# Kernel tuning notes

Measured on AMD Instinct MI355X. Metric: run time of the kernel, lower is better.

The kernel has to match this reference:

```python
import jax, jax.numpy as jnp
import numpy as np

B, N_EX, N_KC, D_E, D_C, D_H = 32, 1024, 128, 64, 64, 64


def setup_inputs() -> dict:
    key = jax.random.key(0)
    ks = jax.random.split(key, 20)
    return {
        "h": jax.random.normal(ks[0], (B, N_KC, D_H), jnp.float32),
        "ex": jax.random.uniform(ks[1], (B, N_EX), jnp.float32),
        "su": jax.random.uniform(ks[2], (B,), jnp.float32),
        "ex_graph": jax.random.uniform(ks[3], (N_EX, N_KC), jnp.float32),
        "kc_gamma": jax.random.normal(ks[4], (N_KC, N_KC), jnp.float32),
        "W_ex": jax.random.normal(ks[5], (D_E, 2 * N_EX), jnp.float32) * 0.02,
        "W_kc": jax.random.normal(ks[6], (D_C, N_KC), jnp.float32) * 0.05,
        "tgru_wih": jax.random.normal(ks[7], (3 * D_H, D_E), jnp.float32) * 0.05,
        "tgru_whh": jax.random.normal(ks[8], (3 * D_H, D_H), jnp.float32) * 0.05,
        "tgru_bih": jax.random.normal(ks[9], (3 * D_H,), jnp.float32) * 0.05,
        "tgru_bhh": jax.random.normal(ks[10], (3 * D_H,), jnp.float32) * 0.05,
        "fpart_w": jax.random.normal(ks[11], (D_H, D_C + D_H), jnp.float32) * 0.05,
        "fpart_b": jax.random.normal(ks[12], (D_H,), jnp.float32) * 0.05,
        "ulin_w": jax.random.normal(ks[13], (D_H, D_H), jnp.float32) * 0.05,
        "ulin_b": jax.random.normal(ks[14], (D_H,), jnp.float32) * 0.05,
        "ugru_wih": jax.random.normal(ks[15], (3 * D_H, D_H), jnp.float32) * 0.05,
        "ugru_whh": jax.random.normal(ks[16], (3 * D_H, D_H), jnp.float32) * 0.05,
        "ugru_bih": jax.random.normal(ks[17], (3 * D_H,), jnp.float32) * 0.05,
        "ugru_bhh": jax.random.normal(ks[18], (3 * D_H,), jnp.float32) * 0.05,
    }


def _gru_cell(x, h, wih, whh, bih, bhh):
    # torch.nn.GRUCell: gates in order r, z, n
    gi = x @ wih.T + bih
    gh = h @ whh.T + bhh
    ir, iz, inn = jnp.split(gi, 3, axis=-1)
    hr, hz, hn = jnp.split(gh, 3, axis=-1)
    r = jax.nn.sigmoid(ir + hr)
    z = jax.nn.sigmoid(iz + hz)
    n = jnp.tanh(inn + r * hn)
    return (1.0 - z) * n + z * h


def reference(h, ex, su, ex_graph, kc_gamma, W_ex, W_kc,
              tgru_wih, tgru_whh, tgru_bih, tgru_bhh,
              fpart_w, fpart_b, ulin_w, ulin_b,
              ugru_wih, ugru_whh, ugru_bih, ugru_bhh):
    bsz, n_kc, d_h = h.shape
    kc_graph = jax.nn.sigmoid(kc_gamma)  # (n_kc, n_kc)

    # exercise embedding from [ex*su, ex*(1-su)]
    x_id = jnp.concatenate([ex * su[:, None], ex * (1.0 - su)[:, None]], axis=-1)  # (B, 2*n_ex)
    x = x_id @ W_ex.T  # (B, d_e)

    kci = ex @ ex_graph  # (B, n_kc)
    kci_flat = kci.reshape(bsz * n_kc, 1)

    # temporal GRU update, gated by kci
    x_rep = jnp.broadcast_to(x[:, None, :], (bsz, n_kc, x.shape[-1])).reshape(bsz * n_kc, -1)
    h_flat = h.reshape(bsz * n_kc, d_h)
    th = _gru_cell(x_rep, h_flat, tgru_wih, tgru_whh, tgru_bih, tgru_bhh)
    new_h = (1.0 - kci_flat) * h_flat + kci_flat * th  # (B*n_kc, d_h)

    delta_h = (new_h - h_flat).reshape(bsz, n_kc, d_h)

    # kc_embeddings(eye(n_kc)) == W_kc.T : (n_kc, d_c)
    e = W_kc.T
    # fpart(concat([delta_h_i, e_j])) split into the two weight blocks
    W_dh = fpart_w[:, :d_h]   # acts on delta_h
    W_e = fpart_w[:, d_h:]    # acts on e
    dpart = delta_h @ W_dh.T                      # (B, n_kc_i, d_h)
    epart = e @ W_e.T + fpart_b                   # (n_kc_j, d_h)
    pre = dpart[:, :, None, :] + epart[None, None, :, :]  # (B, i, j, d_h)
    partij = jax.nn.relu(pre)
    partij = partij * kc_graph[None, :, :, None] * kci[:, :, None, None]
    partj = jnp.sum(partij, axis=1)               # (B, n_kc_j, d_h)

    outj = jax.nn.relu(partj @ ulin_w.T + ulin_b).reshape(bsz * n_kc, d_h)
    kcj = (kci @ kc_graph).reshape(bsz * n_kc, 1)

    uh = _gru_cell(outj, new_h, ugru_wih, ugru_whh, ugru_bih, ugru_bhh)
    h_out = (1.0 - kcj) * new_h + kcj * uh
    return h_out.reshape(bsz, n_kc, d_h)
```

## Files before the change

kernel.cpp:

```cpp
#include <hip/hip_runtime.h>
#include <math.h>

#define NB  32
#define NKC 128
#define DH  64
#define NEX 1024
#define G3  192

#define XOFF    0
#define KCIOFF  2048
#define NHOFF   6144
#define DPOFF   268288

__device__ __forceinline__ float sigf(float x) { return 1.0f / (1.0f + expf(-x)); }
__device__ __forceinline__ float dot4(float4 a, float4 b) {
    return fmaf(a.x, b.x, fmaf(a.y, b.y, fmaf(a.z, b.z, a.w * b.w)));
}

__global__ __launch_bounds__(256) void k0_x(
    const float* __restrict__ ex, const float* __restrict__ su,
    const float* __restrict__ W_ex, float* __restrict__ ws)
{
    int t = threadIdx.x, wave = t >> 6, lane = t & 63;
    int b = blockIdx.x >> 3;
    int dbase = (blockIdx.x & 7) * 8;
    float sub = su[b];
    const float* exb = ex + (size_t)b * NEX;
    float er[16];
    #pragma unroll
    for (int i = 0; i < 16; ++i) er[i] = exb[lane + i * 64];
    #pragma unroll
    for (int p = 0; p < 2; ++p) {
        int d = dbase + wave * 2 + p;
        const float* wr = W_ex + (size_t)d * (2 * NEX);
        float a1 = 0.f, a2 = 0.f;
        #pragma unroll
        for (int i = 0; i < 16; ++i) {
            int k = lane + i * 64;
            a1 = fmaf(er[i], wr[k], a1);
            a2 = fmaf(er[i], wr[NEX + k], a2);
        }
        float v = sub * a1 + (1.0f - sub) * a2;
        #pragma unroll
        for (int off = 32; off; off >>= 1) v += __shfl_down(v, off, 64);
        if (lane == 0) ws[XOFF + b * DH + d] = v;
    }
}

__global__ __launch_bounds__(512) void k1_tgru(
    const float* __restrict__ h, const float* __restrict__ ex,
    const float* __restrict__ ex_graph,
    const float* __restrict__ tgru_wih, const float* __restrict__ tgru_whh,
    const float* __restrict__ tgru_bih, const float* __restrict__ tgru_bhh,
    const float* __restrict__ fpart_w, float* __restrict__ ws)
{
    int t = threadIdx.x, wave = t >> 6, lane = t & 63;
    int b = blockIdx.x >> 3;
    int i0 = (blockIdx.x & 7) * 16;

    __shared__ __align__(16) float whh68[G3 * 36];
    __shared__ __align__(16) float wih68[G3 * 36];
    __shared__ __align__(16) float ht[16 * DH];
    __shared__ __align__(16) float dlt[16 * DH];
    __shared__ __align__(16) float xs[DH];
    __shared__ float kred[512];
    __shared__ float gis[G3];
    __shared__ float bhh3[G3];
    __shared__ float kciL[16];

    {
        int i = t & 15, ks = t >> 4, kb = ks * 32;
        const float* exb = ex + (size_t)b * NEX;
        const float* eg = ex_graph + i0 + i;
        float a = 0.f;
        #pragma unroll 4
        for (int k = 0; k < 32; ++k)
            a = fmaf(exb[kb + k], eg[(size_t)(kb + k) * NKC], a);
        kred[t] = a;
    }
    const float* hb = h + (size_t)(b * NKC + i0) * DH;
    for (int idx = t; idx < 16 * DH; idx += 512) ht[idx] = hb[idx];
    if (t < DH) xs[t] = ws[XOFF + b * DH + t];
    if (t < G3) bhh3[t] = tgru_bhh[t];
    __syncthreads();
    if (t < 16) {
        float s = 0.f;
        #pragma unroll
        for (int r = 0; r < 32; ++r) s += kred[r * 16 + t];
        kciL[t] = s;
        ws[KCIOFF + b * NKC + i0 + t] = s;
    }

    float giA = (t < G3) ? tgru_bih[t] : 0.f;
    float ar[2], az[2], an[2];
    #pragma unroll
    for (int m = 0; m < 2; ++m) {
        ar[m] = bhh3[lane]; az[m] = bhh3[64 + lane]; an[m] = bhh3[128 + lane];
    }
    for (int ch = 0; ch < 2; ++ch) {
        __syncthreads();
        for (int idx = t; idx < G3 * 8; idx += 512) {
            int row = idx >> 3, q = idx & 7;
            *(float4*)&whh68[row * 36 + 4 * q] =
                *(const float4*)&tgru_whh[row * DH + ch * 32 + 4 * q];
            *(float4*)&wih68[row * 36 + 4 * q] =
                *(const float4*)&tgru_wih[row * DH + ch * 32 + 4 * q];
        }
        __syncthreads();
        if (t < G3) {
            #pragma unroll
            for (int q = 0; q < 8; ++q) {
                float4 wv = *(float4*)&wih68[t * 36 + 4 * q];
                float4 xv = *(float4*)&xs[ch * 32 + 4 * q];
                giA += dot4(wv, xv);
            }
        }
        #pragma unroll
        for (int q = 0; q < 8; ++q) {
            float4 wr = *(float4*)&whh68[lane * 36 + 4 * q];
            float4 wz = *(float4*)&whh68[(64 + lane) * 36 + 4 * q];
            float4 wn = *(float4*)&whh68[(128 + lane) * 36 + 4 * q];
            int kb = ch * 32 + 4 * q;
            #pragma unroll
            for (int m = 0; m < 2; ++m) {
                float4 hk = *(float4*)&ht[(wave * 2 + m) * DH + kb];
                ar[m] += dot4(wr, hk);
                az[m] += dot4(wz, hk);
                an[m] += dot4(wn, hk);
            }
        }
    }
    if (t < G3) gis[t] = giA;
    __syncthreads();
    #pragma unroll
    for (int m = 0; m < 2; ++m) {
        int il = wave * 2 + m;
        float hval = ht[il * DH + lane];
        float r = sigf(gis[lane] + ar[m]);
        float z = sigf(gis[64 + lane] + az[m]);
        float n = tanhf(gis[128 + lane] + r * an[m]);
        float th = (1.0f - z) * n + z * hval;
        float kv = kciL[il];
        float nh = (1.0f - kv) * hval + kv * th;
        ws[NHOFF + (size_t)(b * NKC + i0 + il) * DH + lane] = nh;
        dlt[il * DH + lane] = kv * (th - hval);
    }
    __syncthreads();
    float* fw68 = whh68;
    for (int idx = t; idx < 64 * 16; idx += 512) {
        int d = idx >> 4, q = idx & 15;
        *(float4*)&fw68[d * 68 + 4 * q] = *(const float4*)&fpart_w[d * 128 + 4 * q];
    }
    __syncthreads();
    float acc[2] = {0.f, 0.f};
    #pragma unroll
    for (int q = 0; q < 16; ++q) {
        float4 w = *(float4*)&fw68[lane * 68 + 4 * q];
        #pragma unroll
        for (int m = 0; m < 2; ++m) {
            float4 dv = *(float4*)&dlt[(wave * 2 + m) * DH + 4 * q];
            acc[m] += dot4(w, dv);
        }
    }
    float* dptT = wih68;
    __syncthreads();
    #pragma unroll
    for (int m = 0; m < 2; ++m) dptT[lane * 17 + wave * 2 + m] = acc[m];
    __syncthreads();
    for (int idx = t; idx < 1024; idx += 512) {
        int d = idx >> 4, il = idx & 15;
        ws[DPOFF + (size_t)b * 8192 + d * NKC + i0 + il] = dptT[d * 17 + il];
    }
}

__global__ __launch_bounds__(512) void kB_update(
    const float* __restrict__ kc_gamma, const float* __restrict__ W_kc,
    const float* __restrict__ fpart_w, const float* __restrict__ fpart_b,
    const float* __restrict__ ulin_w, const float* __restrict__ ulin_b,
    const float* __restrict__ ugru_wih, const float* __restrict__ ugru_whh,
    const float* __restrict__ ugru_bih, const float* __restrict__ ugru_bhh,
    float* __restrict__ ws, float* __restrict__ out)
{
    int t = threadIdx.x, wave = t >> 6, lane = t & 63;
    int b = blockIdx.x >> 3;
    int j0 = (blockIdx.x & 7) * 16;

    __shared__ __align__(16) float scratch[13888];
    __shared__ __align__(16) float pjS[1024];
    __shared__ __align__(16) float outjS[1024];
    __shared__ __align__(16) float newhS[1024];
    __shared__ __align__(16) float epS[1024];
    __shared__ float kciF[NKC];
    __shared__ float kcjS[16];
    __shared__ float bihS[G3];
    __shared__ float bhhS[G3];

    float* dpT  = scratch;
    float* fw68 = scratch + 8448;
    float* wkT  = scratch + 12800;

    const float* dp = ws + DPOFF + (size_t)b * 8192;
    #pragma unroll
    for (int r = 0; r < 4; ++r) {
        int idx4 = t + r * 512;
        int d = idx4 >> 5, qi = idx4 & 31;
        *(float4*)&dpT[d * 132 + 4 * qi] = *(const float4*)&dp[d * NKC + 4 * qi];
    }
    for (int idx = t; idx < 64 * 16; idx += 512) {
        int d = idx >> 4, q = idx & 15;
        *(float4*)&fw68[d * 68 + 4 * q] =
            *(const float4*)&fpart_w[d * 128 + 64 + 4 * q];
    }
    for (int idx = t; idx < 1024; idx += 512) {
        int c = idx >> 4, jl = idx & 15;
        wkT[jl * 68 + c] = W_kc[(size_t)c * NKC + j0 + jl];
    }
    if (t < 256) {
        const float* nhp = ws + NHOFF + (size_t)(b * NKC + j0) * DH;
        *(float4*)&newhS[t * 4] = *(const float4*)&nhp[t * 4];
    }
    if (t < NKC) kciF[t] = ws[KCIOFF + b * NKC + t];
    if (t < G3) { bihS[t] = ugru_bih[t]; bhhS[t] = ugru_bhh[t]; }
    __syncthreads();
    #pragma unroll
    for (int r = 0; r < 2; ++r) {
        int idx = t + r * 512;
        int jl = idx >> 6, d = idx & 63;
        float a = fpart_b[d];
        #pragma unroll
        for (int q = 0; q < 16; ++q) {
            float4 fv = *(float4*)&fw68[d * 68 + 4 * q];
            float4 wv = *(float4*)&wkT[jl * 68 + 4 * q];
            a += dot4(fv, wv);
        }
        epS[jl * DH + d] = a;
    }
    __syncthreads();
    float* wjT = scratch + 8448;
    for (int idx = t; idx < 2048; idx += 512) {
        int i = idx >> 4, jl = idx & 15;
        wjT[jl * 132 + i] = kciF[i] * sigf(kc_gamma[i * NKC + j0 + jl]);
    }
    __syncthreads();
    if (t < 16) {
        float s = 0.f;
        #pragma unroll
        for (int qi = 0; qi < 32; ++qi) {
            float4 v = *(float4*)&wjT[t * 132 + 4 * qi];
            s += v.x + v.y + v.z + v.w;
        }
        kcjS[t] = s;
    }
    float ep[2], pa[2];
    #pragma unroll
    for (int m = 0; m < 2; ++m) {
        ep[m] = epS[(wave * 2 + m) * DH + lane]; pa[m] = 0.f;
    }
    for (int qi = 0; qi < 32; ++qi) {
        float4 dv = *(float4*)&dpT[lane * 132 + 4 * qi];
        #pragma unroll
        for (int m = 0; m < 2; ++m) {
            float4 wv = *(float4*)&wjT[(wave * 2 + m) * 132 + 4 * qi];
            pa[m] = fmaf(fmaxf(dv.x + ep[m], 0.f), wv.x, pa[m]);
            pa[m] = fmaf(fmaxf(dv.y + ep[m], 0.f), wv.y, pa[m]);
            pa[m] = fmaf(fmaxf(dv.z + ep[m], 0.f), wv.z, pa[m]);
            pa[m] = fmaf(fmaxf(dv.w + ep[m], 0.f), wv.w, pa[m]);
        }
    }
    #pragma unroll
    for (int m = 0; m < 2; ++m) pjS[(wave * 2 + m) * DH + lane] = pa[m];
    __syncthreads();
    float* ul68 = scratch;
    for (int idx = t; idx < 64 * 16; idx += 512) {
        int d = idx >> 4, q = idx & 15;
        *(float4*)&ul68[d * 68 + 4 * q] = *(const float4*)&ulin_w[d * DH + 4 * q];
    }
    float ulb = ulin_b[lane];
    __syncthreads();
    float oa[2] = {ulb, ulb};
    #pragma unroll
    for (int q = 0; q < 16; ++q) {
        float4 uv = *(float4*)&ul68[lane * 68 + 4 * q];
        #pragma unroll
        for (int m = 0; m < 2; ++m) {
            float4 pv = *(float4*)&pjS[(wave * 2 + m) * DH + 4 * q];
            oa[m] += dot4(uv, pv);
        }
    }
    #pragma unroll
    for (int m = 0; m < 2; ++m)
        outjS[(wave * 2 + m) * DH + lane] = fmaxf(oa[m], 0.f);
    float* wih36 = scratch;
    float* whh36 = scratch + 6912;
    float gir[2], giz[2], gin[2], ghr[2], ghz[2], ghn[2];
    #pragma unroll
    for (int m = 0; m < 2; ++m)
        gir[m] = giz[m] = gin[m] = ghr[m] = ghz[m] = ghn[m] = 0.f;
    for (int ch = 0; ch < 2; ++ch) {
        __syncthreads();
        for (int idx = t; idx < G3 * 8; idx += 512) {
            int row = idx >> 3, q = idx & 7;
            *(float4*)&wih36[row * 36 + 4 * q] =
                *(const float4*)&ugru_wih[row * DH + ch * 32 + 4 * q];
            *(float4*)&whh36[row * 36 + 4 * q] =
                *(const float4*)&ugru_whh[row * DH + ch * 32 + 4 * q];
        }
        __syncthreads();
        #pragma unroll
        for (int q = 0; q < 8; ++q) {
            float4 wir = *(float4*)&wih36[lane * 36 + 4 * q];
            float4 wiz = *(float4*)&wih36[(64 + lane) * 36 + 4 * q];
            float4 win = *(float4*)&wih36[(128 + lane) * 36 + 4 * q];
            float4 wwr = *(float4*)&whh36[lane * 36 + 4 * q];
            float4 wwz = *(float4*)&whh36[(64 + lane) * 36 + 4 * q];
            float4 wwn = *(float4*)&whh36[(128 + lane) * 36 + 4 * q];
            int kb = ch * 32 + 4 * q;
            #pragma unroll
            for (int m = 0; m < 2; ++m) {
                int jl = wave * 2 + m;
                float4 ov = *(float4*)&outjS[jl * DH + kb];
                float4 nv = *(float4*)&newhS[jl * DH + kb];
                gir[m] += dot4(wir, ov);
                giz[m] += dot4(wiz, ov);
                gin[m] += dot4(win, ov);
                ghr[m] += dot4(wwr, nv);
                ghz[m] += dot4(wwz, nv);
                ghn[m] += dot4(wwn, nv);
            }
        }
    }
    #pragma unroll
    for (int m = 0; m < 2; ++m) {
        int jl = wave * 2 + m;
        float r = sigf(gir[m] + bihS[lane] + ghr[m] + bhhS[lane]);
        float z = sigf(giz[m] + bihS[64 + lane] + ghz[m] + bhhS[64 + lane]);
        float n = tanhf(gin[m] + bihS[128 + lane] + r * (ghn[m] + bhhS[128 + lane]));
        float nh = newhS[jl * DH + lane];
        float uh = (1.0f - z) * n + z * nh;
        float kj = kcjS[jl];
        out[(size_t)(b * NKC + j0 + jl) * DH + lane] = (1.0f - kj) * nh + kj * uh;
    }
}

extern "C" void kernel_launch(void* const* d_in, const int* in_sizes, int n_in,
                              void* d_out, int out_size, void* d_ws, size_t ws_size,
                              hipStream_t stream) {
    const float* h        = (const float*)d_in[0];
    const float* ex       = (const float*)d_in[1];
    const float* su       = (const float*)d_in[2];
    const float* ex_graph = (const float*)d_in[3];
    const float* kc_gamma = (const float*)d_in[4];
    const float* W_ex     = (const float*)d_in[5];
    const float* W_kc     = (const float*)d_in[6];
    const float* tgru_wih = (const float*)d_in[7];
    const float* tgru_whh = (const float*)d_in[8];
    const float* tgru_bih = (const float*)d_in[9];
    const float* tgru_bhh = (const float*)d_in[10];
    const float* fpart_w  = (const float*)d_in[11];
    const float* fpart_b  = (const float*)d_in[12];
    const float* ulin_w   = (const float*)d_in[13];
    const float* ulin_b   = (const float*)d_in[14];
    const float* ugru_wih = (const float*)d_in[15];
    const float* ugru_whh = (const float*)d_in[16];
    const float* ugru_bih = (const float*)d_in[17];
    const float* ugru_bhh = (const float*)d_in[18];
    float* ws  = (float*)d_ws;
    float* out = (float*)d_out;

    hipLaunchKernelGGL(k0_x, dim3(256), dim3(256), 0, stream,
                       ex, su, W_ex, ws);
    hipLaunchKernelGGL(k1_tgru, dim3(256), dim3(512), 0, stream,
                       h, ex, ex_graph, tgru_wih, tgru_whh, tgru_bih,
                       tgru_bhh, fpart_w, ws);
    hipLaunchKernelGGL(kB_update, dim3(256), dim3(512), 0, stream,
                       kc_gamma, W_kc, fpart_w, fpart_b, ulin_w, ulin_b,
                       ugru_wih, ugru_whh, ugru_bih, ugru_bhh, ws, out);
}
```

Before: 127.0 us.

## Hoist epart computation into k0 and halve block size in GRU kernels

The batch-independent epart projection (W_kc^T times fpart_w's e block plus bias) was recomputed by each of 256 update blocks. It is now computed once by 4 extra blocks in the first kernel and stored in workspace. Separately, k1_tgru and kB_update drop from 512 to 256 threads per block, with each wave handling 4 rows instead of 2. This doubles per-thread register accumulators and gives fewer waves per block, trading latency hiding for more register reuse of the weight loads.

```diff
diff --git a/kernel.cpp b/kernel.cpp
--- a/kernel.cpp
+++ b/kernel.cpp
@@ -9,8 +9,9 @@
 
 #define XOFF    0
 #define KCIOFF  2048
-#define NHOFF   6144
-#define DPOFF   268288
+#define EPOFF   6144
+#define NHOFF   14336
+#define DPOFF   276480
 
 __device__ __forceinline__ float sigf(float x) { return 1.0f / (1.0f + expf(-x)); }
 __device__ __forceinline__ float dot4(float4 a, float4 b) {
@@ -19,35 +20,67 @@
 
 __global__ __launch_bounds__(256) void k0_x(
     const float* __restrict__ ex, const float* __restrict__ su,
-    const float* __restrict__ W_ex, float* __restrict__ ws)
+    const float* __restrict__ W_ex, const float* __restrict__ W_kc,
+    const float* __restrict__ fpart_w, const float* __restrict__ fpart_b,
+    float* __restrict__ ws)
 {
     int t = threadIdx.x, wave = t >> 6, lane = t & 63;
-    int b = blockIdx.x >> 3;
-    int dbase = (blockIdx.x & 7) * 8;
-    float sub = su[b];
-    const float* exb = ex + (size_t)b * NEX;
-    float er[16];
-    #pragma unroll
-    for (int i = 0; i < 16; ++i) er[i] = exb[lane + i * 64];
-    #pragma unroll
-    for (int p = 0; p < 2; ++p) {
-        int d = dbase + wave * 2 + p;
-        const float* wr = W_ex + (size_t)d * (2 * NEX);
-        float a1 = 0.f, a2 = 0.f;
-        #pragma unroll
-        for (int i = 0; i < 16; ++i) {
-            int k = lane + i * 64;
-            a1 = fmaf(er[i], wr[k], a1);
-            a2 = fmaf(er[i], wr[NEX + k], a2);
-        }
-        float v = sub * a1 + (1.0f - sub) * a2;
-        #pragma unroll
-        for (int off = 32; off; off >>= 1) v += __shfl_down(v, off, 64);
-        if (lane == 0) ws[XOFF + b * DH + d] = v;
-    }
-}
-
-__global__ __launch_bounds__(512) void k1_tgru(
+    __shared__ __align__(16) float fw68[64 * 68];
+    __shared__ __align__(16) float wkT[32 * 68];
+
+    if (blockIdx.x < 256) {
+        int b = blockIdx.x >> 3;
+        int dbase = (blockIdx.x & 7) * 8;
+        float sub = su[b];
+        const float* exb = ex + (size_t)b * NEX;
+        float er[16];
+        #pragma unroll
+        for (int i = 0; i < 16; ++i) er[i] = exb[lane + i * 64];
+        #pragma unroll
+        for (int p = 0; p < 2; ++p) {
+            int d = dbase + wave * 2 + p;
+            const float* wr = W_ex + (size_t)d * (2 * NEX);
+            float a1 = 0.f, a2 = 0.f;
+            #pragma unroll
+            for (int i = 0; i < 16; ++i) {
+                int k = lane + i * 64;
+                a1 = fmaf(er[i], wr[k], a1);
+                a2 = fmaf(er[i], wr[NEX + k], a2);
+            }
+            float v = sub * a1 + (1.0f - sub) * a2;
+            #pragma unroll
+            for (int off = 32; off; off >>= 1) v += __shfl_down(v, off, 64);
+            if (lane == 0) ws[XOFF + b * DH + d] = v;
+        }
+    } else {
+        int eb = blockIdx.x - 256;
+        for (int idx = t; idx < 64 * 16; idx += 256) {
+            int d = idx >> 4, q = idx & 15;
+            *(float4*)&fw68[d * 68 + 4 * q] =
+                *(const float4*)&fpart_w[d * 128 + 64 + 4 * q];
+        }
+        for (int idx = t; idx < 2048; idx += 256) {
+            int c = idx >> 5, jl = idx & 31;
+            wkT[jl * 68 + c] = W_kc[(size_t)c * NKC + eb * 32 + jl];
+        }
+        __syncthreads();
+        #pragma unroll
+        for (int r = 0; r < 8; ++r) {
+            int idx = t + r * 256;
+            int jl = idx >> 6, d = idx & 63;
+            float a = fpart_b[d];
+            #pragma unroll
+            for (int q = 0; q < 16; ++q) {
+                float4 fv = *(float4*)&fw68[d * 68 + 4 * q];
+                float4 wv = *(float4*)&wkT[jl * 68 + 4 * q];
+                a += dot4(fv, wv);
+            }
+            ws[EPOFF + (eb * 32 + jl) * DH + d] = a;
+        }
+    }
+}
+
+__global__ __launch_bounds__(256) void k1_tgru(
     const float* __restrict__ h, const float* __restrict__ ex,
     const float* __restrict__ ex_graph,
     const float* __restrict__ tgru_wih, const float* __restrict__ tgru_whh,
@@ -58,72 +91,74 @@
     int b = blockIdx.x >> 3;
     int i0 = (blockIdx.x & 7) * 16;
 
-    __shared__ __align__(16) float whh68[G3 * 36];
-    __shared__ __align__(16) float wih68[G3 * 36];
+    __shared__ __align__(16) float whh36[G3 * 36];
+    __shared__ __align__(16) float wih36[G3 * 36];
     __shared__ __align__(16) float ht[16 * DH];
     __shared__ __align__(16) float dlt[16 * DH];
     __shared__ __align__(16) float xs[DH];
-    __shared__ float kred[512];
+    __shared__ float kred[256];
     __shared__ float gis[G3];
     __shared__ float bhh3[G3];
     __shared__ float kciL[16];
 
     {
-        int i = t & 15, ks = t >> 4, kb = ks * 32;
+        int i = t & 15, ks = t >> 4, kb = ks * 64;
         const float* exb = ex + (size_t)b * NEX;
         const float* eg = ex_graph + i0 + i;
         float a = 0.f;
         #pragma unroll 4
-        for (int k = 0; k < 32; ++k)
+        for (int k = 0; k < 64; ++k)
             a = fmaf(exb[kb + k], eg[(size_t)(kb + k) * NKC], a);
         kred[t] = a;
     }
-    const float* hb = h + (size_t)(b * NKC + i0) * DH;
-    for (int idx = t; idx < 16 * DH; idx += 512) ht[idx] = hb[idx];
+    {
+        const float* hb = h + (size_t)(b * NKC + i0) * DH;
+        *(float4*)&ht[t * 4] = *(const float4*)&hb[t * 4];
+    }
     if (t < DH) xs[t] = ws[XOFF + b * DH + t];
     if (t < G3) bhh3[t] = tgru_bhh[t];
     __syncthreads();
     if (t < 16) {
         float s = 0.f;
         #pragma unroll
-        for (int r = 0; r < 32; ++r) s += kred[r * 16 + t];
+        for (int r = 0; r < 16; ++r) s += kred[r * 16 + t];
         kciL[t] = s;
         ws[KCIOFF + b * NKC + i0 + t] = s;
     }
 
     float giA = (t < G3) ? tgru_bih[t] : 0.f;
-    float ar[2], az[2], an[2];
-    #pragma unroll
-    for (int m = 0; m < 2; ++m) {
+    float ar[4], az[4], an[4];
+    #pragma unroll
+    for (int m = 0; m < 4; ++m) {
         ar[m] = bhh3[lane]; az[m] = bhh3[64 + lane]; an[m] = bhh3[128 + lane];
     }
     for (int ch = 0; ch < 2; ++ch) {
         __syncthreads();
-        for (int idx = t; idx < G3 * 8; idx += 512) {
+        for (int idx = t; idx < G3 * 8; idx += 256) {
             int row = idx >> 3, q = idx & 7;
-            *(float4*)&whh68[row * 36 + 4 * q] =
+            *(float4*)&whh36[row * 36 + 4 * q] =
                 *(const float4*)&tgru_whh[row * DH + ch * 32 + 4 * q];
-            *(float4*)&wih68[row * 36 + 4 * q] =
+            *(float4*)&wih36[row * 36 + 4 * q] =
                 *(const float4*)&tgru_wih[row * DH + ch * 32 + 4 * q];
         }
         __syncthreads();
         if (t < G3) {
             #pragma unroll
             for (int q = 0; q < 8; ++q) {
-                float4 wv = *(float4*)&wih68[t * 36 + 4 * q];
+                float4 wv = *(float4*)&wih36[t * 36 + 4 * q];
                 float4 xv = *(float4*)&xs[ch * 32 + 4 * q];
                 giA += dot4(wv, xv);
             }
         }
         #pragma unroll
         for (int q = 0; q < 8; ++q) {
-            float4 wr = *(float4*)&whh68[lane * 36 + 4 * q];
-            float4 wz = *(float4*)&whh68[(64 + lane) * 36 + 4 * q];
-            float4 wn = *(float4*)&whh68[(128 + lane) * 36 + 4 * q];
+            float4 wr = *(float4*)&whh36[lane * 36 + 4 * q];
+            float4 wz = *(float4*)&whh36[(64 + lane) * 36 + 4 * q];
+            float4 wn = *(float4*)&whh36[(128 + lane) * 36 + 4 * q];
             int kb = ch * 32 + 4 * q;
             #pragma unroll
-            for (int m = 0; m < 2; ++m) {
-                float4 hk = *(float4*)&ht[(wave * 2 + m) * DH + kb];
+            for (int m = 0; m < 4; ++m) {
+                float4 hk = *(float4*)&ht[(wave * 4 + m) * DH + kb];
                 ar[m] += dot4(wr, hk);
                 az[m] += dot4(wz, hk);
                 an[m] += dot4(wn, hk);
@@ -133,8 +168,8 @@
     if (t < G3) gis[t] = giA;
     __syncthreads();
     #pragma unroll
-    for (int m = 0; m < 2; ++m) {
-        int il = wave * 2 + m;
+    for (int m = 0; m < 4; ++m) {
+        int il = wave * 4 + m;
         float hval = ht[il * DH + lane];
         float r = sigf(gis[lane] + ar[m]);
         float z = sigf(gis[64 + lane] + az[m]);
@@ -146,36 +181,35 @@
         dlt[il * DH + lane] = kv * (th - hval);
     }
     __syncthreads();
-    float* fw68 = whh68;
-    for (int idx = t; idx < 64 * 16; idx += 512) {
+    float* fw68 = whh36;
+    for (int idx = t; idx < 64 * 16; idx += 256) {
         int d = idx >> 4, q = idx & 15;
         *(float4*)&fw68[d * 68 + 4 * q] = *(const float4*)&fpart_w[d * 128 + 4 * q];
     }
     __syncthreads();
-    float acc[2] = {0.f, 0.f};
+    float acc[4] = {0.f, 0.f, 0.f, 0.f};
     #pragma unroll
     for (int q = 0; q < 16; ++q) {
         float4 w = *(float4*)&fw68[lane * 68 + 4 * q];
         #pragma unroll
-        for (int m = 0; m < 2; ++m) {
-            float4 dv = *(float4*)&dlt[(wave * 2 + m) * DH + 4 * q];
+        for (int m = 0; m < 4; ++m) {
+            float4 dv = *(float4*)&dlt[(wave * 4 + m) * DH + 4 * q];
             acc[m] += dot4(w, dv);
         }
     }
-    float* dptT = wih68;
-    __syncthreads();
-    #pragma unroll
-    for (int m = 0; m < 2; ++m) dptT[lane * 17 + wave * 2 + m] = acc[m];
-    __syncthreads();
-    for (int idx = t; idx < 1024; idx += 512) {
+    float* dptT = wih36;
+    __syncthreads();
+    #pragma unroll
+    for (int m = 0; m < 4; ++m) dptT[lane * 17 + wave * 4 + m] = acc[m];
+    __syncthreads();
+    for (int idx = t; idx < 1024; idx += 256) {
         int d = idx >> 4, il = idx & 15;
         ws[DPOFF + (size_t)b * 8192 + d * NKC + i0 + il] = dptT[d * 17 + il];
     }
 }
 
-__global__ __launch_bounds__(512) void kB_update(
-    const float* __restrict__ kc_gamma, const float* __restrict__ W_kc,
-    const float* __restrict__ fpart_w, const float* __restrict__ fpart_b,
+__global__ __launch_bounds__(256) void kB_update(
+    const float* __restrict__ kc_gamma,
     const float* __restrict__ ulin_w, const float* __restrict__ ulin_b,
     const float* __restrict__ ugru_wih, const float* __restrict__ ugru_whh,
     const float* __restrict__ ugru_bih, const float* __restrict__ ugru_bhh,
@@ -185,7 +219,7 @@
     int b = blockIdx.x >> 3;
     int j0 = (blockIdx.x & 7) * 16;
 
-    __shared__ __align__(16) float scratch[13888];
+    __shared__ __align__(16) float scratch[13824];
     __shared__ __align__(16) float pjS[1024];
     __shared__ __align__(16) float outjS[1024];
     __shared__ __align__(16) float newhS[1024];
@@ -195,49 +229,23 @@
     __shared__ float bihS[G3];
     __shared__ float bhhS[G3];
 
-    float* dpT  = scratch;
-    float* fw68 = scratch + 8448;
-    float* wkT  = scratch + 12800;
+    float* dpT = scratch;
+    float* wjT = scratch + 8448;
 
     const float* dp = ws + DPOFF + (size_t)b * 8192;
     #pragma unroll
-    for (int r = 0; r < 4; ++r) {
-        int idx4 = t + r * 512;
+    for (int r = 0; r < 8; ++r) {
+        int idx4 = t + r * 256;
         int d = idx4 >> 5, qi = idx4 & 31;
         *(float4*)&dpT[d * 132 + 4 * qi] = *(const float4*)&dp[d * NKC + 4 * qi];
     }
-    for (int idx = t; idx < 64 * 16; idx += 512) {
-        int d = idx >> 4, q = idx & 15;
-        *(float4*)&fw68[d * 68 + 4 * q] =
-            *(const float4*)&fpart_w[d * 128 + 64 + 4 * q];
-    }
-    for (int idx = t; idx < 1024; idx += 512) {
-        int c = idx >> 4, jl = idx & 15;
-        wkT[jl * 68 + c] = W_kc[(size_t)c * NKC + j0 + jl];
-    }
-    if (t < 256) {
-        const float* nhp = ws + NHOFF + (size_t)(b * NKC + j0) * DH;
-        *(float4*)&newhS[t * 4] = *(const float4*)&nhp[t * 4];
-    }
+    *(float4*)&epS[t * 4]   = *(const float4*)&ws[EPOFF + j0 * DH + t * 4];
+    *(float4*)&newhS[t * 4] =
+        *(const float4*)&ws[NHOFF + (size_t)(b * NKC + j0) * DH + t * 4];
     if (t < NKC) kciF[t] = ws[KCIOFF + b * NKC + t];
     if (t < G3) { bihS[t] = ugru_bih[t]; bhhS[t] = ugru_bhh[t]; }
     __syncthreads();
-    #pragma unroll
-    for (int r = 0; r < 2; ++r) {
-        int idx = t + r * 512;
-        int jl = idx >> 6, d = idx & 63;
-        float a = fpart_b[d];
-        #pragma unroll
-        for (int q = 0; q < 16; ++q) {
-            float4 fv = *(float4*)&fw68[d * 68 + 4 * q];
-            float4 wv = *(float4*)&wkT[jl * 68 + 4 * q];
-            a += dot4(fv, wv);
-        }
-        epS[jl * DH + d] = a;
-    }
-    __syncthreads();
-    float* wjT = scratch + 8448;
-    for (int idx = t; idx < 2048; idx += 512) {
+    for (int idx = t; idx < 2048; idx += 256) {
         int i = idx >> 4, jl = idx & 15;
         wjT[jl * 132 + i] = kciF[i] * sigf(kc_gamma[i * NKC + j0 + jl]);
     }
@@ -251,16 +259,16 @@
         }
         kcjS[t] = s;
     }
-    float ep[2], pa[2];
-    #pragma unroll
-    for (int m = 0; m < 2; ++m) {
-        ep[m] = epS[(wave * 2 + m) * DH + lane]; pa[m] = 0.f;
+    float ep[4], pa[4];
+    #pragma unroll
+    for (int m = 0; m < 4; ++m) {
+        ep[m] = epS[(wave * 4 + m) * DH + lane]; pa[m] = 0.f;
     }
     for (int qi = 0; qi < 32; ++qi) {
         float4 dv = *(float4*)&dpT[lane * 132 + 4 * qi];
         #pragma unroll
-        for (int m = 0; m < 2; ++m) {
-            float4 wv = *(float4*)&wjT[(wave * 2 + m) * 132 + 4 * qi];
+        for (int m = 0; m < 4; ++m) {
+            float4 wv = *(float4*)&wjT[(wave * 4 + m) * 132 + 4 * qi];
             pa[m] = fmaf(fmaxf(dv.x + ep[m], 0.f), wv.x, pa[m]);
             pa[m] = fmaf(fmaxf(dv.y + ep[m], 0.f), wv.y, pa[m]);
             pa[m] = fmaf(fmaxf(dv.z + ep[m], 0.f), wv.z, pa[m]);
@@ -268,37 +276,37 @@
         }
     }
     #pragma unroll
-    for (int m = 0; m < 2; ++m) pjS[(wave * 2 + m) * DH + lane] = pa[m];
+    for (int m = 0; m < 4; ++m) pjS[(wave * 4 + m) * DH + lane] = pa[m];
     __syncthreads();
     float* ul68 = scratch;
-    for (int idx = t; idx < 64 * 16; idx += 512) {
+    for (int idx = t; idx < 64 * 16; idx += 256) {
         int d = idx >> 4, q = idx & 15;
         *(float4*)&ul68[d * 68 + 4 * q] = *(const float4*)&ulin_w[d * DH + 4 * q];
     }
     float ulb = ulin_b[lane];
     __syncthreads();
-    float oa[2] = {ulb, ulb};
+    float oa[4] = {ulb, ulb, ulb, ulb};
     #pragma unroll
     for (int q = 0; q < 16; ++q) {
         float4 uv = *(float4*)&ul68[lane * 68 + 4 * q];
         #pragma unroll
-        for (int m = 0; m < 2; ++m) {
-            float4 pv = *(float4*)&pjS[(wave * 2 + m) * DH + 4 * q];
+        for (int m = 0; m < 4; ++m) {
+            float4 pv = *(float4*)&pjS[(wave * 4 + m) * DH + 4 * q];
             oa[m] += dot4(uv, pv);
         }
     }
     #pragma unroll
-    for (int m = 0; m < 2; ++m)
-        outjS[(wave * 2 + m) * DH + lane] = fmaxf(oa[m], 0.f);
+    for (int m = 0; m < 4; ++m)
+        outjS[(wave * 4 + m) * DH + lane] = fmaxf(oa[m], 0.f);
     float* wih36 = scratch;
     float* whh36 = scratch + 6912;
-    float gir[2], giz[2], gin[2], ghr[2], ghz[2], ghn[2];
-    #pragma unroll
-    for (int m = 0; m < 2; ++m)
+    float gir[4], giz[4], gin[4], ghr[4], ghz[4], ghn[4];
+    #pragma unroll
+    for (int m = 0; m < 4; ++m)
         gir[m] = giz[m] = gin[m] = ghr[m] = ghz[m] = ghn[m] = 0.f;
     for (int ch = 0; ch < 2; ++ch) {
         __syncthreads();
-        for (int idx = t; idx < G3 * 8; idx += 512) {
+        for (int idx = t; idx < G3 * 8; idx += 256) {
             int row = idx >> 3, q = idx & 7;
             *(float4*)&wih36[row * 36 + 4 * q] =
                 *(const float4*)&ugru_wih[row * DH + ch * 32 + 4 * q];
@@ -316,8 +324,8 @@
             float4 wwn = *(float4*)&whh36[(128 + lane) * 36 + 4 * q];
             int kb = ch * 32 + 4 * q;
             #pragma unroll
-            for (int m = 0; m < 2; ++m) {
-                int jl = wave * 2 + m;
+            for (int m = 0; m < 4; ++m) {
+                int jl = wave * 4 + m;
                 float4 ov = *(float4*)&outjS[jl * DH + kb];
                 float4 nv = *(float4*)&newhS[jl * DH + kb];
                 gir[m] += dot4(wir, ov);
@@ -330,8 +338,8 @@
         }
     }
     #pragma unroll
-    for (int m = 0; m < 2; ++m) {
-        int jl = wave * 2 + m;
+    for (int m = 0; m < 4; ++m) {
+        int jl = wave * 4 + m;
         float r = sigf(gir[m] + bihS[lane] + ghr[m] + bhhS[lane]);
         float z = sigf(giz[m] + bihS[64 + lane] + ghz[m] + bhhS[64 + lane]);
         float n = tanhf(gin[m] + bihS[128 + lane] + r * (ghn[m] + bhhS[128 + lane]));
@@ -367,12 +375,12 @@
     float* ws  = (float*)d_ws;
     float* out = (float*)d_out;
 
-    hipLaunchKernelGGL(k0_x, dim3(256), dim3(256), 0, stream,
-                       ex, su, W_ex, ws);
-    hipLaunchKernelGGL(k1_tgru, dim3(256), dim3(512), 0, stream,
+    hipLaunchKernelGGL(k0_x, dim3(260), dim3(256), 0, stream,
+                       ex, su, W_ex, W_kc, fpart_w, fpart_b, ws);
+    hipLaunchKernelGGL(k1_tgru, dim3(256), dim3(256), 0, stream,
                        h, ex, ex_graph, tgru_wih, tgru_whh, tgru_bih,
                        tgru_bhh, fpart_w, ws);
-    hipLaunchKernelGGL(kB_update, dim3(256), dim3(512), 0, stream,
-                       kc_gamma, W_kc, fpart_w, fpart_b, ulin_w, ulin_b,
+    hipLaunchKernelGGL(kB_update, dim3(256), dim3(256), 0, stream,
+                       kc_gamma, ulin_w, ulin_b,
                        ugru_wih, ugru_whh, ugru_bih, ugru_bhh, ws, out);
 }
```

New measurement: 142.8 us. 12.4% more time.
